# Kernel optimization log

Hardware: AMD Instinct MI355X
Metric: run time of the kernel (lower is better)

Reference implementation:

```python
import jax, jax.numpy as jnp
import numpy as np

B, S, D, E, R, TOP_K = 4, 4096, 1024, 10, 4, 2
SCALING = 1.0 / R  # alpha / rank


def setup_inputs() -> dict:
    key = jax.random.key(0)
    ks = jax.random.split(key, 7)
    return {
        "x": jax.random.normal(ks[0], (B, S, D), dtype=jnp.float32),
        "W_base": jax.random.normal(ks[1], (D, D), dtype=jnp.float32) * (D ** -0.5),
        "b_base": jax.random.normal(ks[2], (D,), dtype=jnp.float32) * 0.02,
        "gate_W": jax.random.normal(ks[3], (E, D), dtype=jnp.float32) * (D ** -0.5),
        "gate_b": jax.random.normal(ks[4], (E,), dtype=jnp.float32) * 0.02,
        "lora_down": jax.random.normal(ks[5], (E, R, D), dtype=jnp.float32) * (D ** -0.5),
        "lora_up": jax.random.normal(ks[6], (E, D, R), dtype=jnp.float32) * (R ** -0.5),
    }


def reference(x, W_base, b_base, gate_W, gate_b, lora_down, lora_up):
    # Base (frozen) linear: [B,S,D]
    base_out = jnp.einsum("bsd,od->bso", x, W_base) + b_base

    # Top-k gating: logits [B,S,E] -> sparse softmax weights [B,S,E]
    logits = jnp.einsum("bsd,ed->bse", x, gate_W) + gate_b
    top_vals, top_idx = jax.lax.top_k(logits, TOP_K)          # [B,S,K]
    top_w = jax.nn.softmax(top_vals, axis=-1)                 # [B,S,K]
    # scatter top-k weights back to dense [B,S,E] (non-top-k are zero)
    weights = jnp.sum(top_w[..., None] * jax.nn.one_hot(top_idx, E, dtype=x.dtype), axis=-2)

    # All-expert LoRA (matches original loop); weight in rank space to avoid
    # materializing [B,S,E,D]: sum_e w_e * up_e(down_e(x)) * scaling
    h = jnp.einsum("bsd,erd->bser", x, lora_down)             # [B,S,E,R]
    h = h * weights[..., None]
    lora_out = jnp.einsum("bser,edr->bsd", h, lora_up) * SCALING

    return base_out + lora_out
```

## Files before the change

kernel.cpp:

```cpp
#include <hip/hip_runtime.h>
#include <hip/hip_bf16.h>
#include <cstdint>
#include <cstddef>

#define D_DIM 1024
#define E_NUM 10

typedef __attribute__((ext_vector_type(8))) short bf16x8;
typedef __attribute__((ext_vector_type(4))) float f32x4;
typedef unsigned short u16;
typedef unsigned int u32;

__device__ __forceinline__ u16 f2bf(float f) {
  union { float f; u32 u; } v; v.f = f;
  u32 r = v.u + 0x7fffu + ((v.u >> 16) & 1u);
  return (u16)(r >> 16);
}
__device__ __forceinline__ float bf2f(u16 u) {
  union { u32 u; float f; } v; v.u = ((u32)u) << 16; return v.f;
}
__device__ __forceinline__ float dot4(float4 a, float4 b) {
  return a.x * b.x + a.y * b.y + a.z * b.z + a.w * b.w;
}

__global__ void conv_w(const float* __restrict__ W, u16* __restrict__ Wb) {
  const int i = (blockIdx.x * 256 + threadIdx.x) * 8;
  float4 a = *(const float4*)(W + i);
  float4 b = *(const float4*)(W + i + 4);
  *(ushort4*)(Wb + i)     = make_ushort4(f2bf(a.x), f2bf(a.y), f2bf(a.z), f2bf(a.w));
  *(ushort4*)(Wb + i + 4) = make_ushort4(f2bf(b.x), f2bf(b.y), f2bf(b.z), f2bf(b.w));
}

__global__ void prep_ldb(const float* __restrict__ ld, u16* __restrict__ Bld) {
  const int r = blockIdx.x;
  for (int c = threadIdx.x; c < D_DIM; c += 256)
    Bld[r * D_DIM + c] = (r < 40) ? f2bf(ld[r * D_DIM + c]) : (u16)0;
}

__global__ __launch_bounds__(256)
void moe_prep_h(const float* __restrict__ x, const u16* __restrict__ Bld,
                float* __restrict__ h_all, u16* __restrict__ xb) {
  __shared__ u16 sX[4][16 * 64];
  __shared__ u16 sB[4][48 * 64];
  __shared__ float sP[4][3][16][17];

  const int tid = threadIdx.x, lane = tid & 63, w = tid >> 6;
  const int r0 = blockIdx.x * 16;
  const int kbase = w * 256;

  f32x4 acc[3] = {};

  float4 av[4];
#pragma unroll
  for (int i = 0; i < 2; ++i) {
    const int c = lane * 2 + i, row = c >> 3, kc = c & 7;
    const float* g = x + (size_t)(r0 + row) * D_DIM + kbase + kc * 8;
    av[i * 2]     = *(const float4*)g;
    av[i * 2 + 1] = *(const float4*)(g + 4);
  }

#pragma unroll 1
  for (int kt = 0; kt < 4; ++kt) {
    const int k0 = kbase + kt * 64;
#pragma unroll
    for (int i = 0; i < 6; ++i) {
      const int c = i * 64 + lane, row = c >> 3, kc = (c & 7) ^ (row & 7);
      __builtin_amdgcn_global_load_lds(
          (const __attribute__((address_space(1))) u32*)(Bld + (size_t)row * D_DIM + k0 + kc * 8),
          (__attribute__((address_space(3))) u32*)&sB[w][c * 8], 16, 0, 0);
    }
#pragma unroll
    for (int i = 0; i < 2; ++i) {
      const int c = lane * 2 + i, row = c >> 3, kc = c & 7;
      const float4 a = av[i * 2], b = av[i * 2 + 1];
      const ushort4 ha = make_ushort4(f2bf(a.x), f2bf(a.y), f2bf(a.z), f2bf(a.w));
      const ushort4 hb = make_ushort4(f2bf(b.x), f2bf(b.y), f2bf(b.z), f2bf(b.w));
      const int off = (row * 128 + kc * 16) ^ ((row & 7) << 4);
      *(ushort4*)((char*)sX[w] + off)     = ha;
      *(ushort4*)((char*)sX[w] + off + 8) = hb;
      if (xb) {
        u16* dst = xb + (size_t)(r0 + row) * D_DIM + k0 + kc * 8;
        *(ushort4*)dst       = ha;
        *(ushort4*)(dst + 4) = hb;
      }
    }
    __syncthreads();
    if (kt < 3) {
#pragma unroll
      for (int i = 0; i < 2; ++i) {
        const int c = lane * 2 + i, row = c >> 3, kc = c & 7;
        const float* g = x + (size_t)(r0 + row) * D_DIM + (k0 + 64) + kc * 8;
        av[i * 2]     = *(const float4*)g;
        av[i * 2 + 1] = *(const float4*)(g + 4);
      }
    }
#pragma unroll
    for (int kk = 0; kk < 2; ++kk) {
      const int kb = kk * 64 + ((lane >> 4) * 16);
      const int rA = lane & 15;
      const bf16x8 a0 = *(const bf16x8*)((const char*)sX[w] + ((rA * 128 + kb) ^ ((rA & 7) << 4)));
#pragma unroll
      for (int cf = 0; cf < 3; ++cf) {
        const int rB = cf * 16 + (lane & 15);
        const bf16x8 q = *(const bf16x8*)((const char*)sB[w] + ((rB * 128 + kb) ^ ((rB & 7) << 4)));
        acc[cf] = __builtin_amdgcn_mfma_f32_16x16x32_bf16(a0, q, acc[cf], 0, 0, 0);
      }
    }
    __syncthreads();
  }

#pragma unroll
  for (int cf = 0; cf < 3; ++cf)
#pragma unroll
    for (int j = 0; j < 4; ++j)
      sP[w][cf][(lane >> 4) * 4 + j][lane & 15] = acc[cf][j];
  __syncthreads();

  const int row = tid >> 4, c16 = tid & 15;
#pragma unroll
  for (int cf = 0; cf < 3; ++cf) {
    const int col = cf * 16 + c16;
    if (col < 40) {
      const float s = sP[0][cf][row][c16] + sP[1][cf][row][c16] +
                      sP[2][cf][row][c16] + sP[3][cf][row][c16];
      h_all[(size_t)(r0 + row) * 40 + col] = s;
    }
  }
}

__global__ __launch_bounds__(256, 2)
void moe_gate(const float* __restrict__ x, const float* __restrict__ gW,
              const float* __restrict__ gb, const float* __restrict__ h_all,
              int* __restrict__ ids, float* __restrict__ cvals) {
  __shared__ float sgW[E_NUM * D_DIM];
  __shared__ float sgb[16];
  const int tid = threadIdx.x, lane = tid & 63, w = tid >> 6;
  for (int i = tid; i < E_NUM * D_DIM; i += 256) sgW[i] = gW[i];
  if (tid < E_NUM) sgb[tid] = gb[tid];
  __syncthreads();

  const int tb = blockIdx.x * 16 + w * 4;

  float4 xv[4][4];
#pragma unroll
  for (int tok = 0; tok < 4; ++tok)
#pragma unroll
    for (int j = 0; j < 4; ++j)
      xv[tok][j] = *(const float4*)(x + (size_t)(tb + tok) * D_DIM + j * 256 + lane * 4);

  float lg[4][E_NUM];
#pragma unroll
  for (int e = 0; e < E_NUM; ++e) {
    float a0 = 0.f, a1 = 0.f, a2 = 0.f, a3 = 0.f;
#pragma unroll
    for (int j = 0; j < 4; ++j) {
      const float4 wv = *(const float4*)(sgW + e * D_DIM + j * 256 + lane * 4);
      a0 += dot4(xv[0][j], wv);
      a1 += dot4(xv[1][j], wv);
      a2 += dot4(xv[2][j], wv);
      a3 += dot4(xv[3][j], wv);
    }
#pragma unroll
    for (int o = 32; o; o >>= 1) {
      a0 += __shfl_xor(a0, o);
      a1 += __shfl_xor(a1, o);
      a2 += __shfl_xor(a2, o);
      a3 += __shfl_xor(a3, o);
    }
    lg[0][e] = a0 + sgb[e];
    lg[1][e] = a1 + sgb[e];
    lg[2][e] = a2 + sgb[e];
    lg[3][e] = a3 + sgb[e];
  }

  if (lane < 4) {
    const int tok = lane, t = tb + tok;
    int e0 = 0; float v0 = lg[tok][0];
#pragma unroll
    for (int e = 1; e < E_NUM; ++e) if (lg[tok][e] > v0) { v0 = lg[tok][e]; e0 = e; }
    int e1 = -1; float v1 = -3.0e38f;
#pragma unroll
    for (int e = 0; e < E_NUM; ++e) if (e != e0 && lg[tok][e] > v1) { v1 = lg[tok][e]; e1 = e; }
    const float pp = expf(v1 - v0);
    const float inv = 1.f / (1.f + pp);
    const float s0 = inv * 0.25f, s1 = pp * inv * 0.25f;
    ids[t * 2] = e0; ids[t * 2 + 1] = e1;
    const float4 h0 = *(const float4*)(h_all + (size_t)t * 40 + e0 * 4);
    const float4 h1 = *(const float4*)(h_all + (size_t)t * 40 + e1 * 4);
    *(float4*)(cvals + t * 8)     = make_float4(h0.x * s0, h0.y * s0, h0.z * s0, h0.w * s0);
    *(float4*)(cvals + t * 8 + 4) = make_float4(h1.x * s1, h1.y * s1, h1.z * s1, h1.w * s1);
  }
}

__global__ __launch_bounds__(256, 2)
void moe_gemm_bf(const u16* __restrict__ xb, const u16* __restrict__ Wb,
                 const float* __restrict__ bias, const int* __restrict__ ids,
                 const float* __restrict__ cvals, const float* __restrict__ lup,
                 float* __restrict__ out) {
  __shared__ u16 Al[128 * 64];
  __shared__ u16 Bl[128 * 64];

  const int tid = threadIdx.x, lane = tid & 63, wid = tid >> 6;
  const int wm = wid >> 1, wn = wid & 1;
  const int p = blockIdx.x;
  const int cx = p & 7, q = p >> 3;
  const int nb = q & 7, mb = cx * 16 + (q >> 3);
  const int m0 = mb * 128, n0 = nb * 128;

  f32x4 acc[4][4] = {};

#pragma unroll 1
  for (int kt = 0; kt < 16; ++kt) {
    const int k0 = kt * 64;
#pragma unroll
    for (int i = 0; i < 4; ++i) {
      int c = i * 256 + tid, row = c >> 3, kc = (c & 7) ^ (row & 7);
      __builtin_amdgcn_global_load_lds(
          (const __attribute__((address_space(1))) u32*)(xb + (size_t)(m0 + row) * D_DIM + k0 + kc * 8),
          (__attribute__((address_space(3))) u32*)&Al[c * 8], 16, 0, 0);
    }
#pragma unroll
    for (int i = 0; i < 4; ++i) {
      int c = i * 256 + tid, row = c >> 3, kc = (c & 7) ^ (row & 7);
      __builtin_amdgcn_global_load_lds(
          (const __attribute__((address_space(1))) u32*)(Wb + (size_t)(n0 + row) * D_DIM + k0 + kc * 8),
          (__attribute__((address_space(3))) u32*)&Bl[c * 8], 16, 0, 0);
    }
    __syncthreads();
#pragma unroll
    for (int kk = 0; kk < 2; ++kk) {
      bf16x8 af[4], bfr[4];
      const int kb = kk * 64 + ((lane >> 4) * 16);
#pragma unroll
      for (int m = 0; m < 4; ++m) {
        int row = wm * 64 + m * 16 + (lane & 15);
        af[m] = *(const bf16x8*)((const char*)Al + ((row * 128 + kb) ^ ((row & 7) << 4)));
      }
#pragma unroll
      for (int n = 0; n < 4; ++n) {
        int row = wn * 64 + n * 16 + (lane & 15);
        bfr[n] = *(const bf16x8*)((const char*)Bl + ((row * 128 + kb) ^ ((row & 7) << 4)));
      }
#pragma unroll
      for (int m = 0; m < 4; ++m)
#pragma unroll
        for (int n = 0; n < 4; ++n)
          acc[m][n] = __builtin_amdgcn_mfma_f32_16x16x32_bf16(af[m], bfr[n], acc[m][n], 0, 0, 0);
    }
    __syncthreads();
  }

  const int rg = lane >> 4, cl = lane & 15;
  const int baser = m0 + wm * 64, basec = n0 + wn * 64;
  float bs[4];
#pragma unroll
  for (int n = 0; n < 4; ++n) bs[n] = bias[basec + n * 16 + cl];
#pragma unroll
  for (int m = 0; m < 4; ++m)
#pragma unroll
    for (int j = 0; j < 4; ++j) {
      const int rr = baser + m * 16 + rg * 4 + j;
      const int2 id2 = *(const int2*)(ids + rr * 2);
      const float4 c0 = *(const float4*)(cvals + rr * 8);
      const float4 c1 = *(const float4*)(cvals + rr * 8 + 4);
      const float* u0b = lup + (size_t)id2.x * (D_DIM * 4);
      const float* u1b = lup + (size_t)id2.y * (D_DIM * 4);
#pragma unroll
      for (int n = 0; n < 4; ++n) {
        const int cc = basec + n * 16 + cl;
        float4 u0 = *(const float4*)(u0b + cc * 4);
        float4 u1 = *(const float4*)(u1b + cc * 4);
        float v = acc[m][n][j] + bs[n];
        v += c0.x * u0.x + c0.y * u0.y + c0.z * u0.z + c0.w * u0.w;
        v += c1.x * u1.x + c1.y * u1.y + c1.z * u1.z + c1.w * u1.w;
        out[(size_t)rr * D_DIM + cc] = v;
      }
    }
}

__global__ __launch_bounds__(256, 2)
void moe_gemm_f32(const float* __restrict__ x, const u16* __restrict__ Wb,
                  const float* __restrict__ bias, const int* __restrict__ ids,
                  const float* __restrict__ cvals, const float* __restrict__ lup,
                  float* __restrict__ out) {
  __shared__ u16 Al[128 * 64];
  __shared__ u16 Bl[128 * 64];
  const int tid = threadIdx.x, lane = tid & 63, wid = tid >> 6;
  const int wm = wid >> 1, wn = wid & 1;
  const int p = blockIdx.x;
  const int cx = p & 7, q = p >> 3;
  const int nb = q & 7, mb = cx * 16 + (q >> 3);
  const int m0 = mb * 128, n0 = nb * 128;
  f32x4 acc[4][4] = {};
  float4 av[8];
#pragma unroll
  for (int t = 0; t < 8; ++t) {
    int c = t * 256 + tid, row = c >> 4, k4 = c & 15;
    av[t] = *(const float4*)(x + (size_t)(m0 + row) * D_DIM + k4 * 4);
  }
#pragma unroll 1
  for (int kt = 0; kt < 16; ++kt) {
    const int k0 = kt * 64;
#pragma unroll
    for (int i = 0; i < 4; ++i) {
      int c = i * 256 + tid, row = c >> 3, kc = (c & 7) ^ (row & 7);
      __builtin_amdgcn_global_load_lds(
          (const __attribute__((address_space(1))) u32*)(Wb + (size_t)(n0 + row) * D_DIM + k0 + kc * 8),
          (__attribute__((address_space(3))) u32*)&Bl[c * 8], 16, 0, 0);
    }
#pragma unroll
    for (int t = 0; t < 8; ++t) {
      int c = t * 256 + tid, row = c >> 4, k4 = c & 15;
      int off = (row * 128 + k4 * 8) ^ ((row & 7) << 4);
      *(ushort4*)((char*)Al + off) =
          make_ushort4(f2bf(av[t].x), f2bf(av[t].y), f2bf(av[t].z), f2bf(av[t].w));
    }
    __syncthreads();
    if (kt < 15) {
#pragma unroll
      for (int t = 0; t < 8; ++t) {
        int c = t * 256 + tid, row = c >> 4, k4 = c & 15;
        av[t] = *(const float4*)(x + (size_t)(m0 + row) * D_DIM + (k0 + 64) + k4 * 4);
      }
    }
#pragma unroll
    for (int kk = 0; kk < 2; ++kk) {
      bf16x8 af[4], bfr[4];
      const int kb = kk * 64 + ((lane >> 4) * 16);
#pragma unroll
      for (int m = 0; m < 4; ++m) {
        int row = wm * 64 + m * 16 + (lane & 15);
        af[m] = *(const bf16x8*)((const char*)Al + ((row * 128 + kb) ^ ((row & 7) << 4)));
      }
#pragma unroll
      for (int n = 0; n < 4; ++n) {
        int row = wn * 64 + n * 16 + (lane & 15);
        bfr[n] = *(const bf16x8*)((const char*)Bl + ((row * 128 + kb) ^ ((row & 7) << 4)));
      }
#pragma unroll
      for (int m = 0; m < 4; ++m)
#pragma unroll
        for (int n = 0; n < 4; ++n)
          acc[m][n] = __builtin_amdgcn_mfma_f32_16x16x32_bf16(af[m], bfr[n], acc[m][n], 0, 0, 0);
    }
    __syncthreads();
  }
  const int rg = lane >> 4, cl = lane & 15;
  const int baser = m0 + wm * 64, basec = n0 + wn * 64;
  float bs[4];
#pragma unroll
  for (int n = 0; n < 4; ++n) bs[n] = bias[basec + n * 16 + cl];
#pragma unroll
  for (int m = 0; m < 4; ++m)
#pragma unroll
    for (int j = 0; j < 4; ++j) {
      const int rr = baser + m * 16 + rg * 4 + j;
      const int2 id2 = *(const int2*)(ids + rr * 2);
      const float4 c0 = *(const float4*)(cvals + rr * 8);
      const float4 c1 = *(const float4*)(cvals + rr * 8 + 4);
      const float* u0b = lup + (size_t)id2.x * (D_DIM * 4);
      const float* u1b = lup + (size_t)id2.y * (D_DIM * 4);
#pragma unroll
      for (int n = 0; n < 4; ++n) {
        const int cc = basec + n * 16 + cl;
        float4 u0 = *(const float4*)(u0b + cc * 4);
        float4 u1 = *(const float4*)(u1b + cc * 4);
        float v = acc[m][n][j] + bs[n];
        v += c0.x * u0.x + c0.y * u0.y + c0.z * u0.z + c0.w * u0.w;
        v += c1.x * u1.x + c1.y * u1.y + c1.z * u1.z + c1.w * u1.w;
        out[(size_t)rr * D_DIM + cc] = v;
      }
    }
}

extern "C" void kernel_launch(void* const* d_in, const int* in_sizes, int n_in,
                              void* d_out, int out_size, void* d_ws, size_t ws_size,
                              hipStream_t stream) {
  const float* x   = (const float*)d_in[0];
  const float* Wb_ = (const float*)d_in[1];
  const float* bb  = (const float*)d_in[2];
  const float* gW  = (const float*)d_in[3];
  const float* gb  = (const float*)d_in[4];
  const float* ld  = (const float*)d_in[5];
  const float* lup = (const float*)d_in[6];

  char* w = (char*)d_ws;
  u16*   Wbf   = (u16*)w;
  u16*   Bld   = (u16*)(w + 2048ull * 1024);
  int*   ids   = (int*)(w + 2144ull * 1024);
  float* cvals = (float*)(w + 2272ull * 1024);
  float* h_all = (float*)(w + 2784ull * 1024);
  const size_t need_full = (5632ull + 32768ull) * 1024;
  const bool full = ws_size >= need_full;
  u16* xb = full ? (u16*)(w + 5632ull * 1024) : nullptr;

  hipLaunchKernelGGL(conv_w,     dim3(512),  dim3(256), 0, stream, Wb_, Wbf);
  hipLaunchKernelGGL(prep_ldb,   dim3(48),   dim3(256), 0, stream, ld, Bld);
  hipLaunchKernelGGL(moe_prep_h, dim3(1024), dim3(256), 0, stream, x, Bld, h_all, xb);
  hipLaunchKernelGGL(moe_gate,   dim3(1024), dim3(256), 0, stream, x, gW, gb, h_all, ids, cvals);
  if (full)
    hipLaunchKernelGGL(moe_gemm_bf, dim3(1024), dim3(256), 0, stream,
                       xb, Wbf, bb, ids, cvals, lup, (float*)d_out);
  else
    hipLaunchKernelGGL(moe_gemm_f32, dim3(1024), dim3(256), 0, stream,
                       x, Wbf, bb, ids, cvals, lup, (float*)d_out);
}
```

Measured before the change: 118.2 us.

## Double-buffer GEMM LDS tiles and read gate weights directly from global

```diff
diff --git a/kernel.cpp b/kernel.cpp
--- a/kernel.cpp
+++ b/kernel.cpp
@@ -132,13 +132,7 @@
 void moe_gate(const float* __restrict__ x, const float* __restrict__ gW,
               const float* __restrict__ gb, const float* __restrict__ h_all,
               int* __restrict__ ids, float* __restrict__ cvals) {
-  __shared__ float sgW[E_NUM * D_DIM];
-  __shared__ float sgb[16];
   const int tid = threadIdx.x, lane = tid & 63, w = tid >> 6;
-  for (int i = tid; i < E_NUM * D_DIM; i += 256) sgW[i] = gW[i];
-  if (tid < E_NUM) sgb[tid] = gb[tid];
-  __syncthreads();
-
   const int tb = blockIdx.x * 16 + w * 4;
 
   float4 xv[4][4];
@@ -154,7 +148,7 @@
     float a0 = 0.f, a1 = 0.f, a2 = 0.f, a3 = 0.f;
 #pragma unroll
     for (int j = 0; j < 4; ++j) {
-      const float4 wv = *(const float4*)(sgW + e * D_DIM + j * 256 + lane * 4);
+      const float4 wv = *(const float4*)(gW + e * D_DIM + j * 256 + lane * 4);
       a0 += dot4(xv[0][j], wv);
       a1 += dot4(xv[1][j], wv);
       a2 += dot4(xv[2][j], wv);
@@ -167,10 +161,11 @@
       a2 += __shfl_xor(a2, o);
       a3 += __shfl_xor(a3, o);
     }
-    lg[0][e] = a0 + sgb[e];
-    lg[1][e] = a1 + sgb[e];
-    lg[2][e] = a2 + sgb[e];
-    lg[3][e] = a3 + sgb[e];
+    const float be = gb[e];
+    lg[0][e] = a0 + be;
+    lg[1][e] = a1 + be;
+    lg[2][e] = a2 + be;
+    lg[3][e] = a3 + be;
   }
 
   if (lane < 4) {
@@ -193,12 +188,12 @@
 }
 
 __global__ __launch_bounds__(256, 2)
-void moe_gemm_bf(const u16* __restrict__ xb, const u16* __restrict__ Wb,
-                 const float* __restrict__ bias, const int* __restrict__ ids,
-                 const float* __restrict__ cvals, const float* __restrict__ lup,
-                 float* __restrict__ out) {
-  __shared__ u16 Al[128 * 64];
-  __shared__ u16 Bl[128 * 64];
+void moe_gemm_2ph(const u16* __restrict__ xb, const u16* __restrict__ Wb,
+                  const float* __restrict__ bias, const int* __restrict__ ids,
+                  const float* __restrict__ cvals, const float* __restrict__ lup,
+                  float* __restrict__ out) {
+  __shared__ u16 Al[2][128 * 64];
+  __shared__ u16 Bl[2][128 * 64];
 
   const int tid = threadIdx.x, lane = tid & 63, wid = tid >> 6;
   const int wm = wid >> 1, wn = wid & 1;
@@ -207,39 +202,55 @@
   const int nb = q & 7, mb = cx * 16 + (q >> 3);
   const int m0 = mb * 128, n0 = nb * 128;
 
+  const int sc_row[4] = { (0 * 256 + tid) >> 3, (1 * 256 + tid) >> 3,
+                          (2 * 256 + tid) >> 3, (3 * 256 + tid) >> 3 };
+  const int sc_kc[4]  = { ((0 * 256 + tid) & 7) ^ (sc_row[0] & 7),
+                          ((1 * 256 + tid) & 7) ^ (sc_row[1] & 7),
+                          ((2 * 256 + tid) & 7) ^ (sc_row[2] & 7),
+                          ((3 * 256 + tid) & 7) ^ (sc_row[3] & 7) };
+
   f32x4 acc[4][4] = {};
+
+#define STAGE(buf, k0)                                                          \
+  {                                                                             \
+    _Pragma("unroll")                                                           \
+    for (int i = 0; i < 4; ++i) {                                               \
+      const int c = i * 256 + tid;                                              \
+      __builtin_amdgcn_global_load_lds(                                         \
+          (const __attribute__((address_space(1))) u32*)(xb +                   \
+              (size_t)(m0 + sc_row[i]) * D_DIM + (k0) + sc_kc[i] * 8),          \
+          (__attribute__((address_space(3))) u32*)&Al[buf][c * 8], 16, 0, 0);   \
+    }                                                                           \
+    _Pragma("unroll")                                                           \
+    for (int i = 0; i < 4; ++i) {                                               \
+      const int c = i * 256 + tid;                                              \
+      __builtin_amdgcn_global_load_lds(                                         \
+          (const __attribute__((address_space(1))) u32*)(Wb +                   \
+              (size_t)(n0 + sc_row[i]) * D_DIM + (k0) + sc_kc[i] * 8),          \
+          (__attribute__((address_space(3))) u32*)&Bl[buf][c * 8], 16, 0, 0);   \
+    }                                                                           \
+  }
+
+  STAGE(0, 0);
+  __syncthreads();
 
 #pragma unroll 1
   for (int kt = 0; kt < 16; ++kt) {
-    const int k0 = kt * 64;
-#pragma unroll
-    for (int i = 0; i < 4; ++i) {
-      int c = i * 256 + tid, row = c >> 3, kc = (c & 7) ^ (row & 7);
-      __builtin_amdgcn_global_load_lds(
-          (const __attribute__((address_space(1))) u32*)(xb + (size_t)(m0 + row) * D_DIM + k0 + kc * 8),
-          (__attribute__((address_space(3))) u32*)&Al[c * 8], 16, 0, 0);
-    }
-#pragma unroll
-    for (int i = 0; i < 4; ++i) {
-      int c = i * 256 + tid, row = c >> 3, kc = (c & 7) ^ (row & 7);
-      __builtin_amdgcn_global_load_lds(
-          (const __attribute__((address_space(1))) u32*)(Wb + (size_t)(n0 + row) * D_DIM + k0 + kc * 8),
-          (__attribute__((address_space(3))) u32*)&Bl[c * 8], 16, 0, 0);
-    }
-    __syncthreads();
+    const int cur = kt & 1;
+    if (kt < 15) STAGE(cur ^ 1, (kt + 1) * 64);
 #pragma unroll
     for (int kk = 0; kk < 2; ++kk) {
       bf16x8 af[4], bfr[4];
       const int kb = kk * 64 + ((lane >> 4) * 16);
 #pragma unroll
       for (int m = 0; m < 4; ++m) {
-        int row = wm * 64 + m * 16 + (lane & 15);
-        af[m] = *(const bf16x8*)((const char*)Al + ((row * 128 + kb) ^ ((row & 7) << 4)));
+        const int row = wm * 64 + m * 16 + (lane & 15);
+        af[m] = *(const bf16x8*)((const char*)Al[cur] + ((row * 128 + kb) ^ ((row & 7) << 4)));
       }
 #pragma unroll
       for (int n = 0; n < 4; ++n) {
-        int row = wn * 64 + n * 16 + (lane & 15);
-        bfr[n] = *(const bf16x8*)((const char*)Bl + ((row * 128 + kb) ^ ((row & 7) << 4)));
+        const int row = wn * 64 + n * 16 + (lane & 15);
+        bfr[n] = *(const bf16x8*)((const char*)Bl[cur] + ((row * 128 + kb) ^ ((row & 7) << 4)));
       }
 #pragma unroll
       for (int m = 0; m < 4; ++m)
@@ -249,6 +260,7 @@
     }
     __syncthreads();
   }
+#undef STAGE
 
   const int rg = lane >> 4, cl = lane & 15;
   const int baser = m0 + wm * 64, basec = n0 + wn * 64;
@@ -399,7 +411,7 @@
   hipLaunchKernelGGL(moe_prep_h, dim3(1024), dim3(256), 0, stream, x, Bld, h_all, xb);
   hipLaunchKernelGGL(moe_gate,   dim3(1024), dim3(256), 0, stream, x, gW, gb, h_all, ids, cvals);
   if (full)
-    hipLaunchKernelGGL(moe_gemm_bf, dim3(1024), dim3(256), 0, stream,
+    hipLaunchKernelGGL(moe_gemm_2ph, dim3(1024), dim3(256), 0, stream,
                        xb, Wbf, bb, ids, cvals, lup, (float*)d_out);
   else
     hipLaunchKernelGGL(moe_gemm_f32, dim3(1024), dim3(256), 0, stream,
```

Result: slower. 126.5 us (+7.1%).
